# Kernel tuning notes

Measured on AMD Instinct MI355X. Metric: run time of the kernel, lower is better.

Reference implementation:

```python
import jax, jax.numpy as jnp
import numpy as np

NP, P = 5, 5  # number of body parts, joints per part


def _windows(t):
    # (binf, length) for the 6 overlapping temporal windows of sequence()
    h, th = t // 2, t // 3
    return [(0, t), (0, h), (h, t - h), (0, th), (th, th), (2 * th, t - 2 * th)]


def _block(xw):
    # xw: (B, NP, P, L, C) -> Gaussian-embedding blocks (B, NP, L, C+1, C+1)
    B, n, p, L, C = xw.shape
    # smoothing over the P (joint-within-part) axis, as in the original code
    xs = xw.at[:, :, 1:-1].set((xw[:, :, 1:-1] + xw[:, :, :-2] + xw[:, :, 2:]) / 3)
    mu = xs.mean(axis=2)  # (B, NP, L, C)
    # temporally shifted centered slices (shifts over the L axis)
    x0 = xw - mu[:, :, None]                       # (B, NP, P, L, C)
    xm = xw[:, :, :, :-2] - mu[:, :, None, 1:-1]   # (B, NP, P, L-2, C)
    xp = xw[:, :, :, 2:] - mu[:, :, None, 1:-1]    # (B, NP, P, L-2, C)
    outer_mean = lambda a: jnp.einsum('bnptc,bnptd->bntcd', a, a) / p
    cov_mid = (outer_mean(xm) + outer_mean(x0[:, :, :, 1:-1]) + outer_mean(xp)) / 3
    xb = x0[:, :, :, ::L - 1]  # boundary frames 0 and L-1
    cov_b = jnp.einsum('bnptc,bnptd->bntcd', xb, xb) / p
    cov = jnp.zeros((B, n, L, C, C), xw.dtype)
    cov = cov.at[:, :, 1:-1].set(cov_mid)
    cov = cov.at[:, :, ::L - 1].set(cov_b)
    elt00 = cov + mu[..., :, None] * mu[..., None, :]  # cov + mu mu^T
    top = jnp.concatenate([elt00, mu[..., None]], axis=-1)            # (.., C, C+1)
    ones = jnp.ones((B, n, L, 1, 1), xw.dtype)
    bot = jnp.concatenate([mu[..., None, :], ones], axis=-1)          # (.., 1, C+1)
    return jnp.concatenate([top, bot], axis=-2)                        # (.., C+1, C+1)


def setup_inputs() -> dict:
    key = jax.random.key(0)
    x = jax.random.normal(key, (256, 600, 25, 3, 1), dtype=jnp.float32)
    return {"input": x}


def reference(input):
    B, T, J, C, _ = input.shape
    # (B, T, J, C, 1) -> (B, NP, P, T, C)  (matches transpose(1,2).reshape)
    x = jnp.moveaxis(input[..., 0], 1, 2).reshape(B, NP, P, T, C)
    blocks = [_block(x[:, :, :, b:b + L]) for b, L in _windows(T)]
    return jnp.concatenate(blocks, axis=2)  # (B, NP, sum(L_s), C+1, C+1)
```

## Files before the change

kernel.cpp:

```cpp
#include <hip/hip_runtime.h>


#define T_ 600
#define CH_ 100
#define NCH_ 6

typedef float fx4 __attribute__((ext_vector_type(4)));

#define BAR_LDS() do { asm volatile("s_waitcnt lgkmcnt(0)" ::: "memory"); \
                       __builtin_amdgcn_s_barrier(); } while (0)

__global__ __launch_bounds__(512) void gauss_agg_kernel(const float* __restrict__ x,
                                                        float* __restrict__ out) {
    __shared__ float4 lds4[2048];
    float* raw = reinterpret_cast<float*>(lds4);

    int blk = blockIdx.x;
    int ch  = blk % NCH_;
    int b   = blk / NCH_;
    int tc  = ch * CH_;
    int tid = (int)threadIdx.x;

    int vtt1 = -1, vtt2 = -1;
    switch (ch) {
        case 0: vtt1 = 0;   break;
        case 1: vtt1 = 199; break;
        case 2: vtt1 = 200; vtt2 = 299; break;
        case 3: vtt1 = 300; vtt2 = 399; break;
        case 4: vtt1 = 400; break;
        case 5: vtt1 = 599; break;
    }

    {
        const float4* srcv = reinterpret_cast<const float4*>(x + ((size_t)b * T_ + tc) * 75);
        float4* rawv = reinterpret_cast<float4*>(raw);
        #pragma unroll
        for (int i = 0; i < 4; ++i) {
            int e = i * 512 + tid;
            if (e < 1875) rawv[e] = srcv[e];
        }
        if (tid < 150) {
            int rp  = (tid < 75) ? (tc > 0 ? tc - 1 : 0)
                                 : (tc + CH_ < T_ ? tc + CH_ : T_ - 1);
            int col = (tid < 75) ? tid : tid - 75;
            raw[7500 + tid] = x[((size_t)b * T_ + rp) * 75 + col];
        }
    }
    BAR_LDS();

    const float w5[5] = {4.f, 2.f, 3.f, 2.f, 4.f};
    fx4* outf4 = reinterpret_cast<fx4*>(out);

    bool active = (tid < 510);
    float e00=0.f,e01=0.f,e02=0.f,e11=0.f,e12=0.f,e22=0.f,mu0=0.f,mu1=0.f,mu2=0.f;
    if (active) {
        bool isvar = (tid >= 500);
        int n, tt;
        if (!isvar) { n = tid / 100; tt = tc + (tid - n * 100); }
        else if (tid < 505) { n = tid - 500; tt = (vtt1 < 0) ? tc : vtt1; }
        else                { n = tid - 505; tt = (vtt2 < 0) ? tc : vtt2; }
        int tl = tt - tc;

        int midoff = tl * 75 + n * 15;
        const float* rc = &raw[midoff];
        const float* r0 = &raw[(tl == 0)  ? 7500 + n * 15 : midoff - 75];
        const float* r1 = &raw[(tl == 99) ? 7575 + n * 15 : midoff + 75];

        float s0=0.f,s1=0.f,s2=0.f, m0=0.f,m1=0.f,m2=0.f;
        float A00=0.f,A01=0.f,A02=0.f,A11=0.f,A12=0.f,A22=0.f;
        #pragma unroll
        for (int p = 0; p < 5; ++p) {
            float a = rc[p*3+0], c = rc[p*3+1], d = rc[p*3+2];
            s0 += a; s1 += c; s2 += d;
            m0 += w5[p]*a; m1 += w5[p]*c; m2 += w5[p]*d;
            A00 += a*a; A01 += a*c; A02 += a*d;
            A11 += c*c; A12 += c*d; A22 += d*d;
        }
        mu0 = m0*(1.f/15.f); mu1 = m1*(1.f/15.f); mu2 = m2*(1.f/15.f);

        float inv = 0.2f;
        if (!isvar) {
            #pragma unroll
            for (int dstep = 0; dstep < 2; ++dstep) {
                const float* rn = dstep ? r1 : r0;
                #pragma unroll
                for (int p = 0; p < 5; ++p) {
                    float a = rn[p*3+0], c = rn[p*3+1], d = rn[p*3+2];
                    s0 += a; s1 += c; s2 += d;
                    A00 += a*a; A01 += a*c; A02 += a*d;
                    A11 += c*c; A12 += c*d; A22 += d*d;
                }
            }
            inv = 1.f/15.f;
        }

        float mb0 = s0*inv, mb1 = s1*inv, mb2 = s2*inv;
        e00 = A00*inv - 2.f*mu0*mb0 + 2.f*mu0*mu0;
        e01 = A01*inv - mu0*mb1 - mb0*mu1 + 2.f*mu0*mu1;
        e02 = A02*inv - mu0*mb2 - mb0*mu2 + 2.f*mu0*mu2;
        e11 = A11*inv - 2.f*mu1*mb1 + 2.f*mu1*mu1;
        e12 = A12*inv - mu1*mb2 - mb1*mu2 + 2.f*mu1*mu2;
        e22 = A22*inv - 2.f*mu2*mb2 + 2.f*mu2*mu2;
    }
    BAR_LDS();

    if (active) {
        int o4 = tid * 4;
        lds4[o4 + (( 0 + tid) & 3)] = make_float4(e00, e01, e02, mu0);
        lds4[o4 + (( 1 + tid) & 3)] = make_float4(e01, e11, e12, mu1);
        lds4[o4 + (( 2 + tid) & 3)] = make_float4(e02, e12, e22, mu2);
        lds4[o4 + (( 3 + tid) & 3)] = make_float4(mu0, mu1, mu2, 1.f);
    }
    BAR_LDS();

    #pragma unroll
    for (int k = 0; k < 12; ++k) {
        int f = k * 512 + tid;
        if (f < 6000) {
            int sl = f >> 2, pc = f & 3;
            int n  = sl / 300;
            int q  = sl - n * 300;
            int w  = q / 100;
            int tl = q - w * 100;
            int tt = tc + tl;
            bool bd;
            if (w == 0)      bd = (tt == 0) || (tt == 599);
            else if (w == 1) { int r = tt % 300; bd = (r == 0) || (r == 299); }
            else             { int r = tt % 200; bd = (r == 0) || (r == 199); }
            int oi;
            if (!bd)             oi = n * 100 + tl;
            else if (tt == vtt1) oi = 500 + n;
            else                 oi = 505 + n;
            size_t o = ((size_t)(b * 5 + n) * 1800 + w * 600 + tt) * 4 + pc;
            float4 v = lds4[oi * 4 + ((pc + oi) & 3)];
            fx4 nv; nv.x = v.x; nv.y = v.y; nv.z = v.z; nv.w = v.w;
            __builtin_nontemporal_store(nv, &outf4[o]);
        }
    }
}

extern "C" void kernel_launch(void* const* d_in, const int* in_sizes, int n_in,
                              void* d_out, int out_size, void* d_ws, size_t ws_size,
                              hipStream_t stream) {
    const float* x = (const float*)d_in[0];
    float* out = (float*)d_out;
    gauss_agg_kernel<<<256 * NCH_, 512, 0, stream>>>(x, out);
}
```

Measured before the change: 37.97 us.

## Double-buffer two time chunks per block using direct global-to-LDS loads

Each block now handles two adjacent 100-frame chunks instead of one, so the grid is halved. The second chunk's input is prefetched into a second LDS buffer while the first chunk is computed and stored. Input is staged with global_load_lds from one contiguous aligned range that already includes the halo rows, which removes the separate halo load and the register round trip. The cost is twice the LDS per block, which may lower occupancy. Correctness also depends on the vmcnt(8) wait ordering the prefetch loads ahead of the stores.

```diff
diff --git a/kernel.cpp b/kernel.cpp
--- a/kernel.cpp
+++ b/kernel.cpp
@@ -3,24 +3,38 @@
 
 #define T_ 600
 #define CH_ 100
-#define NCH_ 6
 
 typedef float fx4 __attribute__((ext_vector_type(4)));
+typedef const __attribute__((address_space(1))) void* gas_t;
+typedef __attribute__((address_space(3))) void* las_t;
 
 #define BAR_LDS() do { asm volatile("s_waitcnt lgkmcnt(0)" ::: "memory"); \
                        __builtin_amdgcn_s_barrier(); } while (0)
 
-__global__ __launch_bounds__(512) void gauss_agg_kernel(const float* __restrict__ x,
-                                                        float* __restrict__ out) {
-    __shared__ float4 lds4[2048];
+__device__ __forceinline__ void stage_issue(const float* __restrict__ x,
+                                            float4* raw4, int b, int tc,
+                                            int tid, int wv) {
+    int s_row = (tc > 0) ? tc - 1 : 0;
+    int e_row = tc + CH_ + 1; if (e_row > T_) e_row = T_;
+    int r0  = (b * 600 + s_row) * 75;
+    int a0  = r0 & ~3;
+    int nfl = (r0 - a0) + (e_row - s_row) * 75;
+    int n4  = (nfl + 3) >> 2;
+    const float4* srcv = reinterpret_cast<const float4*>(x);
+    int base4 = a0 >> 2;
+    #pragma unroll
+    for (int i = 0; i < 4; ++i) {
+        int e  = i * 512 + tid;
+        int g4 = base4 + ((e < n4) ? e : (n4 - 1));
+        float4* ldst = raw4 + (i * 512 + wv * 64);
+        __builtin_amdgcn_global_load_lds((gas_t)(srcv + g4), (las_t)ldst, 16, 0, 0);
+    }
+}
+
+__device__ __forceinline__ void process_chunk(float4* lds4, fx4* outf4,
+                                              int b, int ch, int tid) {
     float* raw = reinterpret_cast<float*>(lds4);
-
-    int blk = blockIdx.x;
-    int ch  = blk % NCH_;
-    int b   = blk / NCH_;
-    int tc  = ch * CH_;
-    int tid = (int)threadIdx.x;
-
+    int tc = ch * CH_;
     int vtt1 = -1, vtt2 = -1;
     switch (ch) {
         case 0: vtt1 = 0;   break;
@@ -30,26 +44,10 @@
         case 4: vtt1 = 400; break;
         case 5: vtt1 = 599; break;
     }
-
-    {
-        const float4* srcv = reinterpret_cast<const float4*>(x + ((size_t)b * T_ + tc) * 75);
-        float4* rawv = reinterpret_cast<float4*>(raw);
-        #pragma unroll
-        for (int i = 0; i < 4; ++i) {
-            int e = i * 512 + tid;
-            if (e < 1875) rawv[e] = srcv[e];
-        }
-        if (tid < 150) {
-            int rp  = (tid < 75) ? (tc > 0 ? tc - 1 : 0)
-                                 : (tc + CH_ < T_ ? tc + CH_ : T_ - 1);
-            int col = (tid < 75) ? tid : tid - 75;
-            raw[7500 + tid] = x[((size_t)b * T_ + rp) * 75 + col];
-        }
-    }
-    BAR_LDS();
+    int s_row = (tc > 0) ? tc - 1 : 0;
+    int off   = ((b * 600 + s_row) * 75) & 3;
 
     const float w5[5] = {4.f, 2.f, 3.f, 2.f, 4.f};
-    fx4* outf4 = reinterpret_cast<fx4*>(out);
 
     bool active = (tid < 510);
     float e00=0.f,e01=0.f,e02=0.f,e11=0.f,e12=0.f,e22=0.f,mu0=0.f,mu1=0.f,mu2=0.f;
@@ -59,12 +57,11 @@
         if (!isvar) { n = tid / 100; tt = tc + (tid - n * 100); }
         else if (tid < 505) { n = tid - 500; tt = (vtt1 < 0) ? tc : vtt1; }
         else                { n = tid - 505; tt = (vtt2 < 0) ? tc : vtt2; }
-        int tl = tt - tc;
 
-        int midoff = tl * 75 + n * 15;
-        const float* rc = &raw[midoff];
-        const float* r0 = &raw[(tl == 0)  ? 7500 + n * 15 : midoff - 75];
-        const float* r1 = &raw[(tl == 99) ? 7575 + n * 15 : midoff + 75];
+        int midoff = off + (tt - s_row) * 75 + n * 15;
+        const float* rc  = &raw[midoff];
+        const float* r0p = rc - 75;
+        const float* r1p = rc + 75;
 
         float s0=0.f,s1=0.f,s2=0.f, m0=0.f,m1=0.f,m2=0.f;
         float A00=0.f,A01=0.f,A02=0.f,A11=0.f,A12=0.f,A22=0.f;
@@ -82,7 +79,7 @@
         if (!isvar) {
             #pragma unroll
             for (int dstep = 0; dstep < 2; ++dstep) {
-                const float* rn = dstep ? r1 : r0;
+                const float* rn = dstep ? r1p : r0p;
                 #pragma unroll
                 for (int p = 0; p < 5; ++p) {
                     float a = rn[p*3+0], c = rn[p*3+1], d = rn[p*3+2];
@@ -106,10 +103,10 @@
 
     if (active) {
         int o4 = tid * 4;
-        lds4[o4 + (( 0 + tid) & 3)] = make_float4(e00, e01, e02, mu0);
-        lds4[o4 + (( 1 + tid) & 3)] = make_float4(e01, e11, e12, mu1);
-        lds4[o4 + (( 2 + tid) & 3)] = make_float4(e02, e12, e22, mu2);
-        lds4[o4 + (( 3 + tid) & 3)] = make_float4(mu0, mu1, mu2, 1.f);
+        lds4[o4 + ((0 + tid) & 3)] = make_float4(e00, e01, e02, mu0);
+        lds4[o4 + ((1 + tid) & 3)] = make_float4(e01, e11, e12, mu1);
+        lds4[o4 + ((2 + tid) & 3)] = make_float4(e02, e12, e22, mu2);
+        lds4[o4 + ((3 + tid) & 3)] = make_float4(mu0, mu1, mu2, 1.f);
     }
     BAR_LDS();
 
@@ -139,10 +136,36 @@
     }
 }
 
+__global__ __launch_bounds__(512) void gauss_agg_kernel(const float* __restrict__ x,
+                                                        float* __restrict__ out) {
+    __shared__ float4 rawA[2048];
+    __shared__ float4 rawB[2048];
+
+    int blk = blockIdx.x;
+    int j   = blk % 3;
+    int b   = blk / 3;
+    int c0  = 2 * j, c1 = 2 * j + 1;
+    int tid = (int)threadIdx.x;
+    int wv  = tid >> 6;
+    fx4* outf4 = reinterpret_cast<fx4*>(out);
+
+    stage_issue(x, rawA, b, c0 * CH_, tid, wv);
+    __syncthreads();
+
+    stage_issue(x, rawB, b, c1 * CH_, tid, wv);
+
+    process_chunk(rawA, outf4, b, c0, tid);
+
+    asm volatile("s_waitcnt vmcnt(8)" ::: "memory");
+    __builtin_amdgcn_s_barrier();
+
+    process_chunk(rawB, outf4, b, c1, tid);
+}
+
 extern "C" void kernel_launch(void* const* d_in, const int* in_sizes, int n_in,
                               void* d_out, int out_size, void* d_ws, size_t ws_size,
                               hipStream_t stream) {
     const float* x = (const float*)d_in[0];
     float* out = (float*)d_out;
-    gauss_agg_kernel<<<256 * NCH_, 512, 0, stream>>>(x, out);
+    gauss_agg_kernel<<<768, 512, 0, stream>>>(x, out);
 }
```

Measured after the change: 37.60 us. No clear change (-1.0%).
